# Optimization experiments

Measured on AMD Instinct MI355X. Metric: run time of the kernel, lower is better.

The kernel has to match this reference:

```python
import jax, jax.numpy as jnp
import numpy as np

H = 2048      # hidden_size
I = 768       # moe_intermediate_size
E = 32        # num_experts
K = 4         # num_experts_per_tok
B, S = 1, 2048


def setup_inputs() -> dict:
    key = jax.random.key(0)
    k0, k1, k2, k3, k4 = jax.random.split(key, 5)
    return {
        "hidden_states": jax.random.normal(k0, (B, S, H), dtype=jnp.float32),
        "gate_w": jax.random.normal(k1, (E, H), dtype=jnp.float32) * 0.02,
        "Wg": jax.random.normal(k2, (E, H, I), dtype=jnp.float32) * 0.02,
        "Wu": jax.random.normal(k3, (E, H, I), dtype=jnp.float32) * 0.02,
        "Wd": jax.random.normal(k4, (E, I, H), dtype=jnp.float32) * 0.02,
        "top_k": K,
    }


def reference(hidden_states, gate_w, Wg, Wu, Wd, top_k):
    b, s, h = hidden_states.shape
    x = hidden_states.reshape(-1, h)                      # [T, H]
    T = x.shape[0]
    e = gate_w.shape[0]

    # Router: softmax over experts, then top-k and renormalize (norm_topk_prob=True)
    logits = x @ gate_w.T                                 # [T, E]
    probs = jax.nn.softmax(logits, axis=-1)
    w, sel = jax.lax.top_k(probs, top_k)                  # [T, K]
    w = w / jnp.sum(w, axis=-1, keepdims=True)

    # Scatter top-k weights into a dense [T, E] combine matrix
    combine = jnp.zeros((T, e), dtype=x.dtype).at[
        jnp.arange(T)[:, None], sel].add(w)               # [T, E]

    # Expert SiLU-gated MLPs, computed densely for all experts (mirrors the
    # ttnn path that repeats tokens across local experts and masks on combine)
    g = jnp.einsum('th,ehi->eti', x, Wg)                  # [E, T, I]
    u = jnp.einsum('th,ehi->eti', x, Wu)                  # [E, T, I]
    a = jax.nn.silu(g) * u                                # [E, T, I]
    # Fold combine weights in before the down projection to avoid an [E,T,H] temp
    a = a * combine.T[:, :, None]                         # [E, T, I]
    out = jnp.einsum('eti,eih->th', a, Wd)                # [T, H]
    return out.reshape(b, s, h)
```

## Files before the change

kernel.cpp:

```cpp
#include <hip/hip_runtime.h>
#include <cstdint>
#include <cstddef>

#define TDIM 2048
#define HDIM 2048
#define IDIM 768
#define EXP  32
#define TOPK 4
#define TKTOT 8192
#define MAXMETA 96

typedef __attribute__((ext_vector_type(8))) short short8;
typedef __attribute__((ext_vector_type(4))) float f32x4;

constexpr size_t OFF_XBF = 0;
constexpr size_t OFF_ACT = OFF_XBF + (size_t)TDIM * HDIM * 2;
constexpr size_t OFF_LOG = OFF_ACT + (size_t)TKTOT * IDIM * 2;
constexpr size_t OFF_SEL = OFF_LOG + (size_t)TDIM * EXP * 4;
constexpr size_t OFF_WTS = OFF_SEL + (size_t)TDIM * TOPK * 4;
constexpr size_t OFF_STK = OFF_WTS + (size_t)TDIM * TOPK * 4;
constexpr size_t OFF_SW  = OFF_STK + (size_t)TKTOT * 4;
constexpr size_t OFF_INV = OFF_SW  + (size_t)TKTOT * 4;
constexpr size_t OFF_CNT = OFF_INV + (size_t)TDIM * TOPK * 4;
constexpr size_t OFF_CUR = OFF_CNT + EXP * 4;
constexpr size_t OFF_OFS = OFF_CUR + EXP * 4;
constexpr size_t OFF_MET = OFF_OFS + (EXP + 1) * 4;
constexpr size_t OFF_NB  = OFF_MET + MAXMETA * 2 * 4;
constexpr size_t OFF_TMP = (OFF_NB + 4 + 255) & ~(size_t)255;
constexpr size_t TMP_BYTES = (size_t)TKTOT * HDIM * 4;
constexpr size_t WB_BYTES = (size_t)EXP * HDIM * IDIM * 2;
constexpr size_t OFF_WGB = (OFF_TMP + TMP_BYTES + 255) & ~(size_t)255;
constexpr size_t OFF_WUB = OFF_WGB + WB_BYTES;
constexpr size_t OFF_WDB = OFF_WUB + WB_BYTES;
constexpr size_t NEED_BF = OFF_WDB + WB_BYTES;

__device__ __forceinline__ unsigned short f2bf(float f) {
  unsigned u = __float_as_uint(f);
  u = (u + 0x7fffu + ((u >> 16) & 1u)) >> 16;
  return (unsigned short)u;
}
__device__ __forceinline__ unsigned pk2(float a, float b) {
  return (unsigned)f2bf(a) | ((unsigned)f2bf(b) << 16);
}
__device__ __forceinline__ void async16(void* lds, const void* g) {
  __builtin_amdgcn_global_load_lds((const __attribute__((address_space(1))) void*)g,
                                   (__attribute__((address_space(3))) void*)lds, 16, 0, 0);
}

__global__ __launch_bounds__(256) void k_cvt(const float* __restrict__ x,
                                             unsigned short* __restrict__ xb) {
  int i = blockIdx.x * 256 + threadIdx.x;
  const float4* s = (const float4*)x;
  float4 a = s[2 * i], b = s[2 * i + 1];
  uint4 o;
  o.x = pk2(a.x, a.y); o.y = pk2(a.z, a.w);
  o.z = pk2(b.x, b.y); o.w = pk2(b.z, b.w);
  ((uint4*)xb)[i] = o;
}

__global__ __launch_bounds__(256) void k_trw(const float* __restrict__ src,
                                             unsigned short* __restrict__ dst,
                                             int R, int C) {
  __shared__ float sm[64 * 65];
  int t = threadIdx.x;
  int c0 = blockIdx.x * 64, r0 = blockIdx.y * 64;
  size_t base = (size_t)blockIdx.z * R * C;
  const float* s = src + base + (size_t)r0 * C + c0;
#pragma unroll
  for (int p = 0; p < 4; p++) {
    int rl = p * 16 + (t >> 4), cl = (t & 15) * 4;
    float4 v = *(const float4*)(s + (size_t)rl * C + cl);
    float* d = &sm[rl * 65 + cl];
    d[0] = v.x; d[1] = v.y; d[2] = v.z; d[3] = v.w;
  }
  __syncthreads();
  unsigned short* o = dst + base + (size_t)c0 * R + r0;
#pragma unroll
  for (int q = 0; q < 4; q++) {
    int cl = q * 16 + (t >> 4), rq = (t & 15) * 4;
    float v0 = sm[(rq + 0) * 65 + cl], v1 = sm[(rq + 1) * 65 + cl];
    float v2 = sm[(rq + 2) * 65 + cl], v3 = sm[(rq + 3) * 65 + cl];
    uint2 u; u.x = pk2(v0, v1); u.y = pk2(v2, v3);
    *(uint2*)(o + (size_t)cl * R + rq) = u;
  }
}

__global__ __launch_bounds__(256) void k_router(const float* __restrict__ x,
                                                const float* __restrict__ gw,
                                                float* __restrict__ logits) {
  __shared__ float smx[4 * HDIM];
  int tid = threadIdx.x;
  int t0 = blockIdx.x * 4;
  const float4* src = (const float4*)(x + (size_t)t0 * HDIM);
  float4* dst = (float4*)smx;
#pragma unroll
  for (int i = 0; i < 8; i++) dst[i * 256 + tid] = src[i * 256 + tid];
  __syncthreads();
  int e = tid >> 3, sl = tid & 7;
  float acc[4] = {0.f, 0.f, 0.f, 0.f};
  const float* gptr = gw + (size_t)e * HDIM + sl * 256;
#pragma unroll 4
  for (int j = 0; j < 64; j++) {
    float4 g4 = *(const float4*)(gptr + j * 4);
#pragma unroll
    for (int tt = 0; tt < 4; tt++) {
      float4 xa = *(const float4*)&smx[tt * HDIM + sl * 256 + j * 4];
      acc[tt] += g4.x * xa.x + g4.y * xa.y + g4.z * xa.z + g4.w * xa.w;
    }
  }
  __syncthreads();
#pragma unroll
  for (int tt = 0; tt < 4; tt++) smx[(tt * EXP + e) * 8 + sl] = acc[tt];
  __syncthreads();
  if (tid < 128) {
    int tt = tid >> 5, ee = tid & 31;
    float s = 0.f;
#pragma unroll
    for (int q = 0; q < 8; q++) s += smx[(tt * EXP + ee) * 8 + q];
    logits[(size_t)(t0 + tt) * EXP + ee] = s;
  }
}

__global__ __launch_bounds__(256) void k_topk(const float* __restrict__ logits,
                                              int* __restrict__ sel,
                                              float* __restrict__ wts,
                                              int* __restrict__ cnt) {
  int t = blockIdx.x * 256 + threadIdx.x;
  float p[EXP];
  float mx = -1e30f;
#pragma unroll
  for (int e = 0; e < EXP; e++) { p[e] = logits[(size_t)t * EXP + e]; mx = fmaxf(mx, p[e]); }
#pragma unroll
  for (int e = 0; e < EXP; e++) p[e] = __expf(p[e] - mx);
  unsigned used = 0; int si[TOPK]; float sv[TOPK]; float tot = 0.f;
  for (int k = 0; k < TOPK; k++) {
    float bm = -1.f; int bi = 0;
#pragma unroll
    for (int e = 0; e < EXP; e++) {
      bool ok = !((used >> e) & 1) && (p[e] > bm);
      bm = ok ? p[e] : bm;
      bi = ok ? e : bi;
    }
    used |= 1u << bi; si[k] = bi; sv[k] = bm; tot += bm;
  }
  float inv = 1.f / tot;
#pragma unroll
  for (int k = 0; k < TOPK; k++) {
    sel[t * TOPK + k] = si[k];
    wts[t * TOPK + k] = sv[k] * inv;
    atomicAdd(&cnt[si[k]], 1);
  }
}

__global__ void k_scan(const int* __restrict__ cnt, int* __restrict__ offs,
                       int* __restrict__ cur, int* __restrict__ meta,
                       int* __restrict__ nb) {
  if (threadIdx.x == 0 && blockIdx.x == 0) {
    int off = 0, n = 0;
    for (int e = 0; e < EXP; e++) {
      offs[e] = off; cur[e] = off;
      int c = cnt[e];
      for (int r = 0; r < c && n < MAXMETA; r += 128) { meta[n * 2] = e; meta[n * 2 + 1] = r; n++; }
      off += c;
    }
    offs[EXP] = off;
    nb[0] = n;
  }
}

__global__ __launch_bounds__(256) void k_scatter(const int* __restrict__ sel,
                                                 const float* __restrict__ wts,
                                                 int* __restrict__ cur,
                                                 int* __restrict__ stok,
                                                 float* __restrict__ sw,
                                                 int* __restrict__ inv) {
  int t = blockIdx.x * 256 + threadIdx.x;
#pragma unroll
  for (int k = 0; k < TOPK; k++) {
    int e = sel[t * TOPK + k];
    int p = atomicAdd(&cur[e], 1);
    stok[p] = t;
    sw[p] = wts[t * TOPK + k];
    inv[t * TOPK + k] = p;
  }
}

__global__ __launch_bounds__(256, 3) void k_gemm1b(
    const unsigned short* __restrict__ Wgb, const unsigned short* __restrict__ Wub,
    const unsigned short* __restrict__ xb,
    const int* __restrict__ stok, const float* __restrict__ sw,
    const int* __restrict__ cnt, const int* __restrict__ offs,
    const int* __restrict__ meta, const int* __restrict__ nb,
    unsigned short* __restrict__ act) {
  int bid = blockIdx.x;
  if (bid >= nb[0]) return;
  int e = meta[bid * 2], r0 = meta[bid * 2 + 1];
  int pos0 = offs[e] + r0;
  int rows = min(128, cnt[e] - r0);
  int n0 = blockIdx.y * 64;

  __shared__ unsigned short smA[128 * 64];
  __shared__ unsigned short smBg[64 * 64];
  __shared__ unsigned short smBu[64 * 64];
  __shared__ int smTok[128];
  __shared__ float smW[128];

  int tid = threadIdx.x;
  if (tid < 128) {
    int rr = (tid < rows) ? tid : 0;
    smTok[tid] = stok[pos0 + rr];
    smW[tid] = (tid < rows) ? sw[pos0 + tid] : 0.f;
  }
  __syncthreads();

  int lane = tid & 63, w = tid >> 6;
  int waveM = w >> 1, waveN = w & 1;

  const unsigned short* aP[4];
  unsigned short* aD[4];
#pragma unroll
  for (int p = 0; p < 4; p++) {
    int r = p * 32 + w * 8 + (lane >> 3);
    aP[p] = xb + (size_t)smTok[r] * HDIM + (((lane & 7) ^ (r & 7)) << 3);
    aD[p] = &smA[(p * 32 + w * 8) * 64];
  }
  const unsigned short* gP[2]; unsigned short* gD[2];
  const unsigned short* uP[2]; unsigned short* uD[2];
  size_t wbase = (size_t)e * IDIM * HDIM;
#pragma unroll
  for (int p = 0; p < 2; p++) {
    int nr = p * 32 + w * 8 + (lane >> 3);
    size_t go = wbase + (size_t)(n0 + nr) * HDIM + (((lane & 7) ^ (nr & 7)) << 3);
    gP[p] = Wgb + go; uP[p] = Wub + go;
    gD[p] = &smBg[(p * 32 + w * 8) * 64];
    uD[p] = &smBu[(p * 32 + w * 8) * 64];
  }

  f32x4 accG[4][2], accU[4][2];
#pragma unroll
  for (int a = 0; a < 4; a++)
#pragma unroll
    for (int b = 0; b < 2; b++) { accG[a][b] = {0.f,0.f,0.f,0.f}; accU[a][b] = {0.f,0.f,0.f,0.f}; }

  int lm = lane & 15, lq = lane >> 4;

  for (int kt = 0; kt < HDIM / 64; kt++) {
    __syncthreads();
#pragma unroll
    for (int p = 0; p < 4; p++) async16(aD[p], aP[p]);
#pragma unroll
    for (int p = 0; p < 2; p++) async16(gD[p], gP[p]);
#pragma unroll
    for (int p = 0; p < 2; p++) async16(uD[p], uP[p]);
    __syncthreads();
#pragma unroll
    for (int s = 0; s < 2; s++) {
      int kq = s * 4 + lq;
      short8 af[4], bg[2], bu[2];
#pragma unroll
      for (int mt = 0; mt < 4; mt++) {
        int m = waveM * 64 + mt * 16 + lm;
        af[mt] = *(const short8*)&smA[m * 64 + ((kq ^ (m & 7)) << 3)];
      }
#pragma unroll
      for (int nt = 0; nt < 2; nt++) {
        int n = waveN * 32 + nt * 16 + lm;
        int off = n * 64 + ((kq ^ (n & 7)) << 3);
        bg[nt] = *(const short8*)&smBg[off];
        bu[nt] = *(const short8*)&smBu[off];
      }
#pragma unroll
      for (int mt = 0; mt < 4; mt++)
#pragma unroll
        for (int nt = 0; nt < 2; nt++) {
          accG[mt][nt] = __builtin_amdgcn_mfma_f32_16x16x32_bf16(af[mt], bg[nt], accG[mt][nt], 0, 0, 0);
          accU[mt][nt] = __builtin_amdgcn_mfma_f32_16x16x32_bf16(af[mt], bu[nt], accU[mt][nt], 0, 0, 0);
        }
    }
#pragma unroll
    for (int p = 0; p < 4; p++) aP[p] += 64;
#pragma unroll
    for (int p = 0; p < 2; p++) { gP[p] += 64; uP[p] += 64; }
  }

#pragma unroll
  for (int mt = 0; mt < 4; mt++)
#pragma unroll
    for (int nt = 0; nt < 2; nt++) {
      int n = n0 + waveN * 32 + nt * 16 + lm;
#pragma unroll
      for (int i = 0; i < 4; i++) {
        int r = waveM * 64 + mt * 16 + lq * 4 + i;
        if (r < rows) {
          float g = accG[mt][nt][i], u = accU[mt][nt][i];
          float sg = g / (1.f + __expf(-g));
          act[(size_t)(pos0 + r) * IDIM + n] = f2bf(sg * u * smW[r]);
        }
      }
    }
}

__global__ __launch_bounds__(256, 3) void k_gemm2b(
    const unsigned short* __restrict__ Wdb, const unsigned short* __restrict__ act,
    const int* __restrict__ cnt, const int* __restrict__ offs,
    const int* __restrict__ meta, const int* __restrict__ nb,
    float* __restrict__ tmp) {
  int bid = blockIdx.x;
  if (bid >= nb[0]) return;
  int e = meta[bid * 2], r0 = meta[bid * 2 + 1];
  int pos0 = offs[e] + r0;
  int rows = min(128, cnt[e] - r0);
  int n0 = blockIdx.y * 128;

  __shared__ unsigned short smA[128 * 64];
  __shared__ unsigned short smB[128 * 64];

  int tid = threadIdx.x;
  int lane = tid & 63, w = tid >> 6;
  int waveM = w >> 1, waveN = w & 1;

  const unsigned short* aP[4];
  unsigned short* aD[4];
#pragma unroll
  for (int p = 0; p < 4; p++) {
    int r = p * 32 + w * 8 + (lane >> 3);
    int pp = pos0 + r; if (pp > TKTOT - 1) pp = TKTOT - 1;
    aP[p] = act + (size_t)pp * IDIM + (((lane & 7) ^ (r & 7)) << 3);
    aD[p] = &smA[(p * 32 + w * 8) * 64];
  }
  const unsigned short* bP[4]; unsigned short* bD[4];
  size_t wbase = (size_t)e * IDIM * HDIM;
#pragma unroll
  for (int p = 0; p < 4; p++) {
    int nr = p * 32 + w * 8 + (lane >> 3);
    bP[p] = Wdb + wbase + (size_t)(n0 + nr) * IDIM + (((lane & 7) ^ (nr & 7)) << 3);
    bD[p] = &smB[(p * 32 + w * 8) * 64];
  }

  f32x4 acc[4][4];
#pragma unroll
  for (int a = 0; a < 4; a++)
#pragma unroll
    for (int b = 0; b < 4; b++) acc[a][b] = {0.f, 0.f, 0.f, 0.f};

  int lm = lane & 15, lq = lane >> 4;

  for (int kt = 0; kt < IDIM / 64; kt++) {
    __syncthreads();
#pragma unroll
    for (int p = 0; p < 4; p++) async16(aD[p], aP[p]);
#pragma unroll
    for (int p = 0; p < 4; p++) async16(bD[p], bP[p]);
    __syncthreads();
#pragma unroll
    for (int s = 0; s < 2; s++) {
      int kq = s * 4 + lq;
      short8 af[4], bf[4];
#pragma unroll
      for (int mt = 0; mt < 4; mt++) {
        int m = waveM * 64 + mt * 16 + lm;
        af[mt] = *(const short8*)&smA[m * 64 + ((kq ^ (m & 7)) << 3)];
      }
#pragma unroll
      for (int nt = 0; nt < 4; nt++) {
        int n = waveN * 64 + nt * 16 + lm;
        bf[nt] = *(const short8*)&smB[n * 64 + ((kq ^ (n & 7)) << 3)];
      }
#pragma unroll
      for (int mt = 0; mt < 4; mt++)
#pragma unroll
        for (int nt = 0; nt < 4; nt++)
          acc[mt][nt] = __builtin_amdgcn_mfma_f32_16x16x32_bf16(af[mt], bf[nt], acc[mt][nt], 0, 0, 0);
    }
#pragma unroll
    for (int p = 0; p < 4; p++) { aP[p] += 64; bP[p] += 64; }
  }

#pragma unroll
  for (int mt = 0; mt < 4; mt++)
#pragma unroll
    for (int nt = 0; nt < 4; nt++) {
      int n = n0 + waveN * 64 + nt * 16 + lm;
#pragma unroll
      for (int i = 0; i < 4; i++) {
        int r = waveM * 64 + mt * 16 + lq * 4 + i;
        if (r < rows) tmp[(size_t)(pos0 + r) * HDIM + n] = acc[mt][nt][i];
      }
    }
}

__global__ __launch_bounds__(256, 2) void k_gemm1(
    const float* __restrict__ Wg, const float* __restrict__ Wu,
    const unsigned short* __restrict__ xb,
    const int* __restrict__ stok, const float* __restrict__ sw,
    const int* __restrict__ cnt, const int* __restrict__ offs,
    const int* __restrict__ meta, const int* __restrict__ nb,
    unsigned short* __restrict__ act) {
  int bid = blockIdx.x;
  if (bid >= nb[0]) return;
  int e = meta[bid * 2 + 0];
  int r0 = meta[bid * 2 + 1];
  int pos0 = offs[e] + r0;
  int rows = min(128, cnt[e] - r0);
  int n0 = blockIdx.y * 128;

  __shared__ unsigned short smA[128 * 64];
  __shared__ unsigned short smBg[128 * 64];
  __shared__ unsigned short smBu[128 * 64];
  __shared__ int smTok[128];
  __shared__ float smW[128];

  int tid = threadIdx.x;
  if (tid < 128) {
    int r = tid;
    int rr = (r < rows) ? r : 0;
    smTok[r] = stok[pos0 + rr];
    smW[r] = (r < rows) ? sw[pos0 + r] : 0.f;
  }
  __syncthreads();

  int lane = tid & 63, w = tid >> 6;
  int waveM = w >> 1, waveN = w & 1;

  const unsigned short* aP[4];
  unsigned short* aD[4];
#pragma unroll
  for (int p = 0; p < 4; p++) {
    int r = p * 32 + w * 8 + (lane >> 3);
    aP[p] = xb + (size_t)smTok[r] * HDIM + (((lane & 7) ^ (r & 7)) << 3);
    aD[p] = &smA[(p * 32 + w * 8) * 64];
  }
  int bn = tid & 127, kh = tid >> 7;
  const float* pG = Wg + (size_t)e * HDIM * IDIM + (size_t)(kh * 32) * IDIM + n0 + bn;
  const float* pU = Wu + (size_t)e * HDIM * IDIM + (size_t)(kh * 32) * IDIM + n0 + bn;

  f32x4 accG[4][4], accU[4][4];
#pragma unroll
  for (int a = 0; a < 4; a++)
#pragma unroll
    for (int b = 0; b < 4; b++) { accG[a][b] = {0.f,0.f,0.f,0.f}; accU[a][b] = {0.f,0.f,0.f,0.f}; }

  int lm = lane & 15, lq = lane >> 4;

  for (int kt = 0; kt < HDIM / 64; kt++) {
    __syncthreads();
#pragma unroll
    for (int p = 0; p < 4; p++) async16(aD[p], aP[p]);
    {
      const float* q = pG; float v[32];
#pragma unroll
      for (int j = 0; j < 32; j++) { v[j] = *q; q += IDIM; }
#pragma unroll
      for (int jj = 0; jj < 4; jj++) {
        short8 o;
#pragma unroll
        for (int z = 0; z < 8; z++) o[z] = (short)f2bf(v[jj * 8 + z]);
        int ck = kh * 4 + jj;
        *(short8*)&smBg[bn * 64 + ((ck ^ (bn & 7)) << 3)] = o;
      }
    }
    {
      const float* q = pU; float v[32];
#pragma unroll
      for (int j = 0; j < 32; j++) { v[j] = *q; q += IDIM; }
#pragma unroll
      for (int jj = 0; jj < 4; jj++) {
        short8 o;
#pragma unroll
        for (int z = 0; z < 8; z++) o[z] = (short)f2bf(v[jj * 8 + z]);
        int ck = kh * 4 + jj;
        *(short8*)&smBu[bn * 64 + ((ck ^ (bn & 7)) << 3)] = o;
      }
    }
    __syncthreads();
#pragma unroll
    for (int s = 0; s < 2; s++) {
      int kq = s * 4 + lq;
      short8 af[4], bg[4], bu[4];
#pragma unroll
      for (int mt = 0; mt < 4; mt++) {
        int m = waveM * 64 + mt * 16 + lm;
        af[mt] = *(const short8*)&smA[m * 64 + ((kq ^ (m & 7)) << 3)];
      }
#pragma unroll
      for (int nt = 0; nt < 4; nt++) {
        int n = waveN * 64 + nt * 16 + lm;
        int off = n * 64 + ((kq ^ (n & 7)) << 3);
        bg[nt] = *(const short8*)&smBg[off];
        bu[nt] = *(const short8*)&smBu[off];
      }
#pragma unroll
      for (int mt = 0; mt < 4; mt++)
#pragma unroll
        for (int nt = 0; nt < 4; nt++) {
          accG[mt][nt] = __builtin_amdgcn_mfma_f32_16x16x32_bf16(af[mt], bg[nt], accG[mt][nt], 0, 0, 0);
          accU[mt][nt] = __builtin_amdgcn_mfma_f32_16x16x32_bf16(af[mt], bu[nt], accU[mt][nt], 0, 0, 0);
        }
    }
#pragma unroll
    for (int p = 0; p < 4; p++) aP[p] += 64;
    pG += (size_t)64 * IDIM;
    pU += (size_t)64 * IDIM;
  }

#pragma unroll
  for (int mt = 0; mt < 4; mt++)
#pragma unroll
    for (int nt = 0; nt < 4; nt++) {
      int n = n0 + waveN * 64 + nt * 16 + lm;
#pragma unroll
      for (int i = 0; i < 4; i++) {
        int r = waveM * 64 + mt * 16 + lq * 4 + i;
        if (r < rows) {
          float g = accG[mt][nt][i], u = accU[mt][nt][i];
          float sg = g / (1.f + __expf(-g));
          act[(size_t)(pos0 + r) * IDIM + n] = f2bf(sg * u * smW[r]);
        }
      }
    }
}

__global__ __launch_bounds__(256, 2) void k_gemm2(
    const float* __restrict__ Wd, const unsigned short* __restrict__ act,
    const int* __restrict__ stok, const int* __restrict__ cnt,
    const int* __restrict__ offs, const int* __restrict__ meta,
    const int* __restrict__ nb, float* __restrict__ dst, int mode) {
  int bid = blockIdx.x;
  if (bid >= nb[0]) return;
  int e = meta[bid * 2 + 0];
  int r0 = meta[bid * 2 + 1];
  int pos0 = offs[e] + r0;
  int rows = min(128, cnt[e] - r0);
  int n0 = blockIdx.y * 128;

  __shared__ unsigned short smA[128 * 64];
  __shared__ unsigned short smB[128 * 64];
  __shared__ int smTok[128];

  int tid = threadIdx.x;
  if (tid < 128) {
    int r = tid;
    int rr = (r < rows) ? r : 0;
    smTok[r] = stok[pos0 + rr];
  }
  __syncthreads();

  int lane = tid & 63, w = tid >> 6;
  int waveM = w >> 1, waveN = w & 1;

  const unsigned short* aP[4];
  unsigned short* aD[4];
#pragma unroll
  for (int p = 0; p < 4; p++) {
    int r = p * 32 + w * 8 + (lane >> 3);
    int pp = pos0 + r; if (pp > TKTOT - 1) pp = TKTOT - 1;
    aP[p] = act + (size_t)pp * IDIM + (((lane & 7) ^ (r & 7)) << 3);
    aD[p] = &smA[(p * 32 + w * 8) * 64];
  }
  int bn = tid & 127, kh = tid >> 7;
  const float* pD = Wd + (size_t)e * IDIM * HDIM + (size_t)(kh * 32) * HDIM + n0 + bn;

  f32x4 acc[4][4];
#pragma unroll
  for (int a = 0; a < 4; a++)
#pragma unroll
    for (int b = 0; b < 4; b++) acc[a][b] = {0.f, 0.f, 0.f, 0.f};

  int lm = lane & 15, lq = lane >> 4;

  for (int kt = 0; kt < IDIM / 64; kt++) {
    __syncthreads();
#pragma unroll
    for (int p = 0; p < 4; p++) async16(aD[p], aP[p]);
    {
      const float* q = pD; float v[32];
#pragma unroll
      for (int j = 0; j < 32; j++) { v[j] = *q; q += HDIM; }
#pragma unroll
      for (int jj = 0; jj < 4; jj++) {
        short8 o;
#pragma unroll
        for (int z = 0; z < 8; z++) o[z] = (short)f2bf(v[jj * 8 + z]);
        int ck = kh * 4 + jj;
        *(short8*)&smB[bn * 64 + ((ck ^ (bn & 7)) << 3)] = o;
      }
    }
    __syncthreads();
#pragma unroll
    for (int s = 0; s < 2; s++) {
      int kq = s * 4 + lq;
      short8 af[4], bf[4];
#pragma unroll
      for (int mt = 0; mt < 4; mt++) {
        int m = waveM * 64 + mt * 16 + lm;
        af[mt] = *(const short8*)&smA[m * 64 + ((kq ^ (m & 7)) << 3)];
      }
#pragma unroll
      for (int nt = 0; nt < 4; nt++) {
        int n = waveN * 64 + nt * 16 + lm;
        bf[nt] = *(const short8*)&smB[n * 64 + ((kq ^ (n & 7)) << 3)];
      }
#pragma unroll
      for (int mt = 0; mt < 4; mt++)
#pragma unroll
        for (int nt = 0; nt < 4; nt++)
          acc[mt][nt] = __builtin_amdgcn_mfma_f32_16x16x32_bf16(af[mt], bf[nt], acc[mt][nt], 0, 0, 0);
    }
#pragma unroll
    for (int p = 0; p < 4; p++) aP[p] += 64;
    pD += (size_t)64 * HDIM;
  }

#pragma unroll
  for (int mt = 0; mt < 4; mt++)
#pragma unroll
    for (int nt = 0; nt < 4; nt++) {
      int n = n0 + waveN * 64 + nt * 16 + lm;
#pragma unroll
      for (int i = 0; i < 4; i++) {
        int r = waveM * 64 + mt * 16 + lq * 4 + i;
        if (r < rows) {
          float val = acc[mt][nt][i];
          if (mode == 0) {
            dst[(size_t)(pos0 + r) * HDIM + n] = val;
          } else {
            __hip_atomic_fetch_add(&dst[(size_t)smTok[r] * HDIM + n], val,
                                   __ATOMIC_RELAXED, __HIP_MEMORY_SCOPE_AGENT);
          }
        }
      }
    }
}

__global__ __launch_bounds__(256) void k_reduce(const float* __restrict__ tmp,
                                                const int* __restrict__ inv,
                                                float* __restrict__ out) {
  int u = blockIdx.x * 256 + threadIdx.x;
  int t = u >> 9, c = u & 511;
  int i0 = inv[t * 4 + 0], i1 = inv[t * 4 + 1], i2 = inv[t * 4 + 2], i3 = inv[t * 4 + 3];
  float4 a = *(const float4*)(tmp + (size_t)i0 * HDIM + c * 4);
  float4 b = *(const float4*)(tmp + (size_t)i1 * HDIM + c * 4);
  float4 d = *(const float4*)(tmp + (size_t)i2 * HDIM + c * 4);
  float4 e = *(const float4*)(tmp + (size_t)i3 * HDIM + c * 4);
  float4 s;
  s.x = a.x + b.x + d.x + e.x;
  s.y = a.y + b.y + d.y + e.y;
  s.z = a.z + b.z + d.z + e.z;
  s.w = a.w + b.w + d.w + e.w;
  *(float4*)(out + (size_t)t * HDIM + c * 4) = s;
}

extern "C" void kernel_launch(void* const* d_in, const int* in_sizes, int n_in,
                              void* d_out, int out_size, void* d_ws, size_t ws_size,
                              hipStream_t stream) {
  const float* x  = (const float*)d_in[0];
  const float* gw = (const float*)d_in[1];
  const float* Wg = (const float*)d_in[2];
  const float* Wu = (const float*)d_in[3];
  const float* Wd = (const float*)d_in[4];
  float* out = (float*)d_out;

  char* ws = (char*)d_ws;
  unsigned short* xb  = (unsigned short*)(ws + OFF_XBF);
  unsigned short* act = (unsigned short*)(ws + OFF_ACT);
  float* logits = (float*)(ws + OFF_LOG);
  int*   sel    = (int*)(ws + OFF_SEL);
  float* wts    = (float*)(ws + OFF_WTS);
  int*   stok   = (int*)(ws + OFF_STK);
  float* sw     = (float*)(ws + OFF_SW);
  int*   inv    = (int*)(ws + OFF_INV);
  int*   cnt    = (int*)(ws + OFF_CNT);
  int*   cur    = (int*)(ws + OFF_CUR);
  int*   offs   = (int*)(ws + OFF_OFS);
  int*   meta   = (int*)(ws + OFF_MET);
  int*   nb     = (int*)(ws + OFF_NB);
  float* tmp    = (float*)(ws + OFF_TMP);
  unsigned short* Wgb = (unsigned short*)(ws + OFF_WGB);
  unsigned short* Wub = (unsigned short*)(ws + OFF_WUB);
  unsigned short* Wdb = (unsigned short*)(ws + OFF_WDB);

  bool useTmp = ws_size >= OFF_TMP + TMP_BYTES;
  bool useBF  = ws_size >= NEED_BF;

  hipMemsetAsync(cnt, 0, EXP * 4, stream);
  k_cvt<<<(TDIM * HDIM / 8) / 256, 256, 0, stream>>>(x, xb);
  k_router<<<TDIM / 4, 256, 0, stream>>>(x, gw, logits);
  k_topk<<<TDIM / 256, 256, 0, stream>>>(logits, sel, wts, cnt);
  k_scan<<<1, 64, 0, stream>>>(cnt, offs, cur, meta, nb);
  k_scatter<<<TDIM / 256, 256, 0, stream>>>(sel, wts, cur, stok, sw, inv);

  if (useBF) {
    k_trw<<<dim3(IDIM / 64, HDIM / 64, EXP), 256, 0, stream>>>(Wg, Wgb, HDIM, IDIM);
    k_trw<<<dim3(IDIM / 64, HDIM / 64, EXP), 256, 0, stream>>>(Wu, Wub, HDIM, IDIM);
    k_trw<<<dim3(HDIM / 64, IDIM / 64, EXP), 256, 0, stream>>>(Wd, Wdb, IDIM, HDIM);
    k_gemm1b<<<dim3(MAXMETA, IDIM / 64), 256, 0, stream>>>(Wgb, Wub, xb, stok, sw, cnt, offs, meta, nb, act);
    k_gemm2b<<<dim3(MAXMETA, HDIM / 128), 256, 0, stream>>>(Wdb, act, cnt, offs, meta, nb, tmp);
    k_reduce<<<(TDIM * 512) / 256, 256, 0, stream>>>(tmp, inv, out);
  } else {
    k_gemm1<<<dim3(MAXMETA, IDIM / 128), 256, 0, stream>>>(Wg, Wu, xb, stok, sw, cnt, offs, meta, nb, act);
    if (useTmp) {
      k_gemm2<<<dim3(MAXMETA, HDIM / 128), 256, 0, stream>>>(Wd, act, stok, cnt, offs, meta, nb, tmp, 0);
      k_reduce<<<(TDIM * 512) / 256, 256, 0, stream>>>(tmp, inv, out);
    } else {
      hipMemsetAsync(out, 0, (size_t)TDIM * HDIM * 4, stream);
      k_gemm2<<<dim3(MAXMETA, HDIM / 128), 256, 0, stream>>>(Wd, act, stok, cnt, offs, meta, nb, out, 1);
    }
  }
}
```

Baseline: 827.9 us.

## Double-buffer LDS tiles in expert GEMMs, parallelize scan, widen transpose stores

Both grouped expert GEMM kernels now use two LDS buffers, so the async global-to-LDS copy for the next K-tile is issued before the MFMA work on the current tile, with one barrier per iteration instead of two. This is meant to hide load latency behind compute, but it doubles LDS use, and the occupancy hint drops from 3 to 2 blocks per CU. The single-thread scan is replaced by a 32-lane wave shuffle prefix sum. The weight transpose kernel now writes 16-byte stores instead of 8-byte ones.

Result: slower. 926.6 us (+11.9%).

```diff
diff --git a/kernel.cpp b/kernel.cpp
--- a/kernel.cpp
+++ b/kernel.cpp
@@ -76,12 +76,15 @@
   __syncthreads();
   unsigned short* o = dst + base + (size_t)c0 * R + r0;
 #pragma unroll
-  for (int q = 0; q < 4; q++) {
-    int cl = q * 16 + (t >> 4), rq = (t & 15) * 4;
+  for (int q = 0; q < 2; q++) {
+    int cl = q * 32 + (t >> 3), rq = (t & 7) * 8;
     float v0 = sm[(rq + 0) * 65 + cl], v1 = sm[(rq + 1) * 65 + cl];
     float v2 = sm[(rq + 2) * 65 + cl], v3 = sm[(rq + 3) * 65 + cl];
-    uint2 u; u.x = pk2(v0, v1); u.y = pk2(v2, v3);
-    *(uint2*)(o + (size_t)cl * R + rq) = u;
+    float v4 = sm[(rq + 4) * 65 + cl], v5 = sm[(rq + 5) * 65 + cl];
+    float v6 = sm[(rq + 6) * 65 + cl], v7 = sm[(rq + 7) * 65 + cl];
+    uint4 u;
+    u.x = pk2(v0, v1); u.y = pk2(v2, v3); u.z = pk2(v4, v5); u.w = pk2(v6, v7);
+    *(uint4*)(o + (size_t)cl * R + rq) = u;
   }
 }
 
@@ -155,16 +158,24 @@
 __global__ void k_scan(const int* __restrict__ cnt, int* __restrict__ offs,
                        int* __restrict__ cur, int* __restrict__ meta,
                        int* __restrict__ nb) {
-  if (threadIdx.x == 0 && blockIdx.x == 0) {
-    int off = 0, n = 0;
-    for (int e = 0; e < EXP; e++) {
-      offs[e] = off; cur[e] = off;
-      int c = cnt[e];
-      for (int r = 0; r < c && n < MAXMETA; r += 128) { meta[n * 2] = e; meta[n * 2 + 1] = r; n++; }
-      off += c;
-    }
-    offs[EXP] = off;
-    nb[0] = n;
+  int l = threadIdx.x;
+  if (l < 32) {
+    int c = cnt[l];
+    int nbl = (c + 127) >> 7;
+    int pc = c, pb = nbl;
+#pragma unroll
+    for (int d = 1; d < 32; d <<= 1) {
+      int vc = __shfl_up(pc, d);
+      int vb = __shfl_up(pb, d);
+      if (l >= d) { pc += vc; pb += vb; }
+    }
+    int offc = pc - c, offb = pb - nbl;
+    offs[l] = offc; cur[l] = offc;
+    if (l == 31) { offs[32] = pc; nb[0] = pb; }
+    for (int r = 0; r < nbl; r++) {
+      meta[(offb + r) * 2] = l;
+      meta[(offb + r) * 2 + 1] = r * 128;
+    }
   }
 }
 
@@ -185,7 +196,7 @@
   }
 }
 
-__global__ __launch_bounds__(256, 3) void k_gemm1b(
+__global__ __launch_bounds__(256, 2) void k_gemm1b(
     const unsigned short* __restrict__ Wgb, const unsigned short* __restrict__ Wub,
     const unsigned short* __restrict__ xb,
     const int* __restrict__ stok, const float* __restrict__ sw,
@@ -199,41 +210,31 @@
   int rows = min(128, cnt[e] - r0);
   int n0 = blockIdx.y * 64;
 
-  __shared__ unsigned short smA[128 * 64];
-  __shared__ unsigned short smBg[64 * 64];
-  __shared__ unsigned short smBu[64 * 64];
-  __shared__ int smTok[128];
-  __shared__ float smW[128];
+  __shared__ unsigned short smA[2 * 128 * 64];
+  __shared__ unsigned short smBg[2 * 64 * 64];
+  __shared__ unsigned short smBu[2 * 64 * 64];
 
   int tid = threadIdx.x;
-  if (tid < 128) {
-    int rr = (tid < rows) ? tid : 0;
-    smTok[tid] = stok[pos0 + rr];
-    smW[tid] = (tid < rows) ? sw[pos0 + tid] : 0.f;
-  }
-  __syncthreads();
-
   int lane = tid & 63, w = tid >> 6;
   int waveM = w >> 1, waveN = w & 1;
 
   const unsigned short* aP[4];
-  unsigned short* aD[4];
+  int aOff[4];
 #pragma unroll
   for (int p = 0; p < 4; p++) {
     int r = p * 32 + w * 8 + (lane >> 3);
-    aP[p] = xb + (size_t)smTok[r] * HDIM + (((lane & 7) ^ (r & 7)) << 3);
-    aD[p] = &smA[(p * 32 + w * 8) * 64];
-  }
-  const unsigned short* gP[2]; unsigned short* gD[2];
-  const unsigned short* uP[2]; unsigned short* uD[2];
+    int rr = (r < rows) ? r : 0;
+    aP[p] = xb + (size_t)stok[pos0 + rr] * HDIM + (((lane & 7) ^ (r & 7)) << 3);
+    aOff[p] = (p * 32 + w * 8) * 64;
+  }
+  const unsigned short* gP[2]; const unsigned short* uP[2]; int bOff[2];
   size_t wbase = (size_t)e * IDIM * HDIM;
 #pragma unroll
   for (int p = 0; p < 2; p++) {
     int nr = p * 32 + w * 8 + (lane >> 3);
     size_t go = wbase + (size_t)(n0 + nr) * HDIM + (((lane & 7) ^ (nr & 7)) << 3);
     gP[p] = Wgb + go; uP[p] = Wub + go;
-    gD[p] = &smBg[(p * 32 + w * 8) * 64];
-    uD[p] = &smBu[(p * 32 + w * 8) * 64];
+    bOff[p] = (p * 32 + w * 8) * 64;
   }
 
   f32x4 accG[4][2], accU[4][2];
@@ -244,15 +245,32 @@
 
   int lm = lane & 15, lq = lane >> 4;
 
+#pragma unroll
+  for (int p = 0; p < 4; p++) async16(&smA[aOff[p]], aP[p]);
+#pragma unroll
+  for (int p = 0; p < 2; p++) { async16(&smBg[bOff[p]], gP[p]); async16(&smBu[bOff[p]], uP[p]); }
+#pragma unroll
+  for (int p = 0; p < 4; p++) aP[p] += 64;
+#pragma unroll
+  for (int p = 0; p < 2; p++) { gP[p] += 64; uP[p] += 64; }
+  __syncthreads();
+
   for (int kt = 0; kt < HDIM / 64; kt++) {
-    __syncthreads();
-#pragma unroll
-    for (int p = 0; p < 4; p++) async16(aD[p], aP[p]);
-#pragma unroll
-    for (int p = 0; p < 2; p++) async16(gD[p], gP[p]);
-#pragma unroll
-    for (int p = 0; p < 2; p++) async16(uD[p], uP[p]);
-    __syncthreads();
+    int cur = kt & 1, nxt = cur ^ 1;
+    if (kt + 1 < HDIM / 64) {
+      int nb_ = nxt * 128 * 64, nbB = nxt * 64 * 64;
+#pragma unroll
+      for (int p = 0; p < 4; p++) async16(&smA[nb_ + aOff[p]], aP[p]);
+#pragma unroll
+      for (int p = 0; p < 2; p++) { async16(&smBg[nbB + bOff[p]], gP[p]); async16(&smBu[nbB + bOff[p]], uP[p]); }
+#pragma unroll
+      for (int p = 0; p < 4; p++) aP[p] += 64;
+#pragma unroll
+      for (int p = 0; p < 2; p++) { gP[p] += 64; uP[p] += 64; }
+    }
+    const unsigned short* A = &smA[cur * 128 * 64];
+    const unsigned short* Bg = &smBg[cur * 64 * 64];
+    const unsigned short* Bu = &smBu[cur * 64 * 64];
 #pragma unroll
     for (int s = 0; s < 2; s++) {
       int kq = s * 4 + lq;
@@ -260,14 +278,14 @@
 #pragma unroll
       for (int mt = 0; mt < 4; mt++) {
         int m = waveM * 64 + mt * 16 + lm;
-        af[mt] = *(const short8*)&smA[m * 64 + ((kq ^ (m & 7)) << 3)];
+        af[mt] = *(const short8*)&A[m * 64 + ((kq ^ (m & 7)) << 3)];
       }
 #pragma unroll
       for (int nt = 0; nt < 2; nt++) {
         int n = waveN * 32 + nt * 16 + lm;
         int off = n * 64 + ((kq ^ (n & 7)) << 3);
-        bg[nt] = *(const short8*)&smBg[off];
-        bu[nt] = *(const short8*)&smBu[off];
+        bg[nt] = *(const short8*)&Bg[off];
+        bu[nt] = *(const short8*)&Bu[off];
       }
 #pragma unroll
       for (int mt = 0; mt < 4; mt++)
@@ -277,10 +295,7 @@
           accU[mt][nt] = __builtin_amdgcn_mfma_f32_16x16x32_bf16(af[mt], bu[nt], accU[mt][nt], 0, 0, 0);
         }
     }
-#pragma unroll
-    for (int p = 0; p < 4; p++) aP[p] += 64;
-#pragma unroll
-    for (int p = 0; p < 2; p++) { gP[p] += 64; uP[p] += 64; }
+    __syncthreads();
   }
 
 #pragma unroll
@@ -294,13 +309,13 @@
         if (r < rows) {
           float g = accG[mt][nt][i], u = accU[mt][nt][i];
           float sg = g / (1.f + __expf(-g));
-          act[(size_t)(pos0 + r) * IDIM + n] = f2bf(sg * u * smW[r]);
+          act[(size_t)(pos0 + r) * IDIM + n] = f2bf(sg * u * sw[pos0 + r]);
         }
       }
     }
 }
 
-__global__ __launch_bounds__(256, 3) void k_gemm2b(
+__global__ __launch_bounds__(256, 2) void k_gemm2b(
     const unsigned short* __restrict__ Wdb, const unsigned short* __restrict__ act,
     const int* __restrict__ cnt, const int* __restrict__ offs,
     const int* __restrict__ meta, const int* __restrict__ nb,
@@ -312,29 +327,27 @@
   int rows = min(128, cnt[e] - r0);
   int n0 = blockIdx.y * 128;
 
-  __shared__ unsigned short smA[128 * 64];
-  __shared__ unsigned short smB[128 * 64];
+  __shared__ unsigned short smA[2 * 128 * 64];
+  __shared__ unsigned short smB[2 * 128 * 64];
 
   int tid = threadIdx.x;
   int lane = tid & 63, w = tid >> 6;
   int waveM = w >> 1, waveN = w & 1;
 
-  const unsigned short* aP[4];
-  unsigned short* aD[4];
+  const unsigned short* aP[4]; int aOff[4];
 #pragma unroll
   for (int p = 0; p < 4; p++) {
     int r = p * 32 + w * 8 + (lane >> 3);
     int pp = pos0 + r; if (pp > TKTOT - 1) pp = TKTOT - 1;
     aP[p] = act + (size_t)pp * IDIM + (((lane & 7) ^ (r & 7)) << 3);
-    aD[p] = &smA[(p * 32 + w * 8) * 64];
-  }
-  const unsigned short* bP[4]; unsigned short* bD[4];
+    aOff[p] = (p * 32 + w * 8) * 64;
+  }
+  const unsigned short* bP[4];
   size_t wbase = (size_t)e * IDIM * HDIM;
 #pragma unroll
   for (int p = 0; p < 4; p++) {
     int nr = p * 32 + w * 8 + (lane >> 3);
     bP[p] = Wdb + wbase + (size_t)(n0 + nr) * IDIM + (((lane & 7) ^ (nr & 7)) << 3);
-    bD[p] = &smB[(p * 32 + w * 8) * 64];
   }
 
   f32x4 acc[4][4];
@@ -345,13 +358,23 @@
 
   int lm = lane & 15, lq = lane >> 4;
 
+#pragma unroll
+  for (int p = 0; p < 4; p++) { async16(&smA[aOff[p]], aP[p]); async16(&smB[aOff[p]], bP[p]); }
+#pragma unroll
+  for (int p = 0; p < 4; p++) { aP[p] += 64; bP[p] += 64; }
+  __syncthreads();
+
   for (int kt = 0; kt < IDIM / 64; kt++) {
-    __syncthreads();
-#pragma unroll
-    for (int p = 0; p < 4; p++) async16(aD[p], aP[p]);
-#pragma unroll
-    for (int p = 0; p < 4; p++) async16(bD[p], bP[p]);
-    __syncthreads();
+    int cur = kt & 1, nxt = cur ^ 1;
+    if (kt + 1 < IDIM / 64) {
+      int nb_ = nxt * 128 * 64;
+#pragma unroll
+      for (int p = 0; p < 4; p++) { async16(&smA[nb_ + aOff[p]], aP[p]); async16(&smB[nb_ + aOff[p]], bP[p]); }
+#pragma unroll
+      for (int p = 0; p < 4; p++) { aP[p] += 64; bP[p] += 64; }
+    }
+    const unsigned short* A = &smA[cur * 128 * 64];
+    const unsigned short* B = &smB[cur * 128 * 64];
 #pragma unroll
     for (int s = 0; s < 2; s++) {
       int kq = s * 4 + lq;
@@ -359,12 +382,12 @@
 #pragma unroll
       for (int mt = 0; mt < 4; mt++) {
         int m = waveM * 64 + mt * 16 + lm;
-        af[mt] = *(const short8*)&smA[m * 64 + ((kq ^ (m & 7)) << 3)];
+        af[mt] = *(const short8*)&A[m * 64 + ((kq ^ (m & 7)) << 3)];
       }
 #pragma unroll
       for (int nt = 0; nt < 4; nt++) {
         int n = waveN * 64 + nt * 16 + lm;
-        bf[nt] = *(const short8*)&smB[n * 64 + ((kq ^ (n & 7)) << 3)];
+        bf[nt] = *(const short8*)&B[n * 64 + ((kq ^ (n & 7)) << 3)];
       }
 #pragma unroll
       for (int mt = 0; mt < 4; mt++)
@@ -372,8 +395,7 @@
         for (int nt = 0; nt < 4; nt++)
           acc[mt][nt] = __builtin_amdgcn_mfma_f32_16x16x32_bf16(af[mt], bf[nt], acc[mt][nt], 0, 0, 0);
     }
-#pragma unroll
-    for (int p = 0; p < 4; p++) { aP[p] += 64; bP[p] += 64; }
+    __syncthreads();
   }
 
 #pragma unroll
```
